# Kernel optimization log

Measured on AMD Instinct MI355X. Metric: run time of the kernel, lower is better.

## Reference

```python
import jax, jax.numpy as jnp
import numpy as np
import math

N_HEAD = 12
N_EMBD = 768

def setup_inputs() -> dict:
    key = jax.random.key(0)
    ks = jax.random.split(key, 5)
    B, T, C = 4, 2048, N_EMBD
    s_attn = 1.0 / math.sqrt(C)
    return {
        "x": jax.random.normal(ks[0], (B, T, C), jnp.float32),
        "w_attn": jax.random.normal(ks[1], (C, 3 * C), jnp.float32) * s_attn,
        "b_attn": jnp.zeros((3 * C,), jnp.float32),
        "w_proj": jax.random.normal(ks[2], (C, C), jnp.float32) * s_attn,
        "b_proj": jnp.zeros((C,), jnp.float32),
    }

def reference(x, w_attn, b_attn, w_proj, b_proj):
    B, T, C = x.shape
    H = N_HEAD
    D = C // H
    qkv = x @ w_attn + b_attn  # [B,T,3C]
    q, k, v = jnp.split(qkv, 3, axis=-1)
    # [B,T,C] -> [B,H,T,D]
    q = q.reshape(B, T, H, D).transpose(0, 2, 1, 3)
    k = k.reshape(B, T, H, D).transpose(0, 2, 1, 3)
    v = v.reshape(B, T, H, D).transpose(0, 2, 1, 3)
    att = jnp.einsum('bhqd,bhkd->bhqk', q, k) * (1.0 / math.sqrt(D))
    causal = jnp.tril(jnp.ones((T, T), bool))
    att = jnp.where(causal[None, None], att, -jnp.inf)
    att = jax.nn.softmax(att, axis=-1)
    y = jnp.einsum('bhqk,bhkd->bhqd', att, v)  # [B,H,T,D]
    y = y.transpose(0, 2, 1, 3).reshape(B, T, C)
    return y @ w_proj + b_proj
```

## Files before the change

kernel.cpp:

```cpp
#include <hip/hip_runtime.h>
#include <hip/hip_bf16.h>

typedef unsigned short u16;
typedef __attribute__((ext_vector_type(4))) short bf16x4;
typedef __attribute__((ext_vector_type(8))) short bf16x8;
typedef __attribute__((ext_vector_type(4))) float f32x4;
typedef __attribute__((ext_vector_type(16))) float f32x16;

#define NB_ 4
#define NT_ 2048
#define NC_ 768
#define NH_ 12
#define ND_ 64
#define NM_ (NB_*NT_)
#define KC_ 24

#define SCQ_ 0.18033688011112042f

__device__ __forceinline__ u16 f2bf(float f){
  union { float f; unsigned u; } c; c.f = f;
  unsigned u = c.u;
  return (u16)((u + 0x7fffu + ((u>>16)&1u)) >> 16);
}

__device__ __forceinline__ unsigned pkbf(float a, float b){
  __hip_bfloat162 h = __float22bfloat162_rn(make_float2(a,b));
  union { __hip_bfloat162 h; unsigned u; } c; c.h = h; return c.u;
}

__device__ __forceinline__ f32x16 mfma32(bf16x8 a, bf16x8 b, f32x16 c){
  return __builtin_amdgcn_mfma_f32_32x32x16_bf16(a, b, c, 0, 0, 0);
}

__device__ __forceinline__ void gload_lds16(const void* g, void* l){
  __builtin_amdgcn_global_load_lds(
    (const __attribute__((address_space(1))) void*)g,
    (__attribute__((address_space(3))) void*)l, 16, 0, 0);
}


__global__ __launch_bounds__(256) void cast_f32_bf16_k(
    const float* __restrict__ in, u16* __restrict__ out, int n4){
  int i = blockIdx.x*256 + threadIdx.x;
  if (i >= n4) return;
  float4 v = ((const float4*)in)[i];
  int row = i / (NC_/4), k4 = (i % (NC_/4))*4;
  size_t off = (((size_t)(row>>7)*KC_ + (k4>>5))*4 + ((k4>>3)&3))*1024 + (row&127)*8 + (k4&7);
  bf16x4 o;
  o[0]=(short)f2bf(v.x); o[1]=(short)f2bf(v.y);
  o[2]=(short)f2bf(v.z); o[3]=(short)f2bf(v.w);
  *(bf16x4*)(out + off) = o;
}

__global__ __launch_bounds__(256) void transpose_cast_k(
    const float* __restrict__ in, u16* __restrict__ out, int R, int Cc){
  __shared__ float tile[32][33];
  int tx = threadIdx.x, ty = threadIdx.y;
  int c0 = blockIdx.x*32, r0 = blockIdx.y*32;
  #pragma unroll
  for (int j=0;j<32;j+=8) tile[ty+j][tx] = in[(size_t)(r0+ty+j)*Cc + c0+tx];
  __syncthreads();
  #pragma unroll
  for (int j=0;j<32;j+=8){
    int n = c0+ty+j, k = r0+tx;
    size_t off = (((size_t)(n>>8)*KC_ + (k>>5))*4 + ((k>>3)&3))*2048 + (n&255)*8 + (k&7);
    out[off] = f2bf(tile[tx][ty+j]);
  }
}

template<int MODE>
__global__ __launch_bounds__(256,2) void gemm256(
  const u16* __restrict__ A, const u16* __restrict__ BT, const float* __restrict__ bias,
  u16* __restrict__ qo, u16* __restrict__ ko, u16* __restrict__ vo,
  float* __restrict__ fo)
{
  __shared__ u16 lds[2][4096 + 8192];
  const int t = threadIdx.x, w = t>>6, l = t&63;
  const int lq = l&31, h = l>>5;
  const int NXB = (MODE==0) ? 9 : 3;
  const int nwg = 64*NXB;
  int sw = (blockIdx.x & 7)*(nwg>>3) + (blockIdx.x >> 3);
  const int rb = sw / NXB, nb = sw % NXB;
  const int brow = rb*128, bcol = nb*256;
  const int wc = w*64;

  f32x16 acc[4][2];
  #pragma unroll
  for (int i=0;i<4;i++)
    #pragma unroll
    for (int j=0;j<2;j++)
      #pragma unroll
      for (int r=0;r<16;r++) acc[i][j][r] = 0.f;

  auto stage = [&](int buf, int kc){
    const u16* Ag = A  + ((size_t)(rb*KC_ + kc))*4096;
    const u16* Bg = BT + ((size_t)(nb*KC_ + kc))*8192;
    char* La = (char*)&lds[buf][0];
    char* Lb = (char*)&lds[buf][4096];
    #pragma unroll
    for (int it=0; it<2; ++it)
      gload_lds16(Ag + (it*256+t)*8, La + (it*256+t)*16);
    #pragma unroll
    for (int it=0; it<4; ++it)
      gload_lds16(Bg + (it*256+t)*8, Lb + (it*256+t)*16);
  };

  stage(0,0);
  __syncthreads();
  int cur = 0;
  for (int kc=0; kc<KC_; ++kc){
    if (kc+1 < KC_) stage(cur^1, kc+1);
    const u16* La = &lds[cur][0];
    const u16* Lb = &lds[cur][4096];
    #pragma unroll
    for (int ks=0; ks<2; ++ks){
      bf16x8 af[4], bfr[2];
      #pragma unroll
      for (int mi=0;mi<4;mi++)
        af[mi] = *(const bf16x8*)(La + ((2*ks+h)*128 + mi*32 + lq)*8);
      #pragma unroll
      for (int nj=0;nj<2;nj++)
        bfr[nj] = *(const bf16x8*)(Lb + ((2*ks+h)*256 + wc + nj*32 + lq)*8);
      __builtin_amdgcn_s_setprio(1);
      #pragma unroll
      for (int mi=0;mi<4;mi++)
        #pragma unroll
        for (int nj=0;nj<2;nj++)
          acc[mi][nj] = mfma32(af[mi], bfr[nj], acc[mi][nj]);
      __builtin_amdgcn_s_setprio(0);
    }
    __syncthreads();
    cur ^= 1;
  }

  if (MODE == 1){
    #pragma unroll
    for (int nj=0;nj<2;nj++){
      int n = bcol + wc + nj*32 + lq;
      float bs = bias[n];
      #pragma unroll
      for (int mi=0;mi<4;mi++)
        #pragma unroll
        for (int r=0;r<16;r++){
          int m = brow + mi*32 + (r&3) + 8*(r>>2) + 4*h;
          fo[(size_t)m*NC_ + n] = acc[mi][nj][r] + bs;
        }
    }
  } else {
    const int sec = nb/3;
    u16* outp = (sec==0) ? qo : (sec==1 ? ko : vo);
    #pragma unroll
    for (int nj=0;nj<2;nj++){
      int n = bcol + wc + nj*32 + lq;
      int cc = n - sec*NC_;
      int hd = cc >> 6, d = cc & 63;
      float bs = bias[n];
      #pragma unroll
      for (int mi=0;mi<4;mi++)
        #pragma unroll
        for (int r=0;r<16;r++){
          int m = brow + mi*32 + (r&3) + 8*(r>>2) + 4*h;
          int bb = m >> 11, tt = m & 2047;
          float v = acc[mi][nj][r] + bs;
          if (sec == 0) v *= SCQ_;
          size_t bhbase = ((size_t)bb*NH_ + hd)*((size_t)NT_*ND_);
          size_t off;
          if (sec == 0){
            off = bhbase + (size_t)tt*ND_ + d;
          } else if (sec == 1){
            off = bhbase + (size_t)(tt>>6)*4096 + (size_t)(d>>3)*512 + (tt&63)*8 + (d&7);
          } else {
            int p = (tt & ~15) | (h<<3) | (r&3) | (((r>>2)&1)<<2);
            off = bhbase + (size_t)(p>>6)*4096 + (size_t)((p&63)>>3)*512 + d*8 + (p&7);
          }
          outp[off] = f2bf(v);
        }
    }
  }
}

__global__ __launch_bounds__(256,4) void attn_kernel(
    const u16* __restrict__ qg, const u16* __restrict__ kg,
    const u16* __restrict__ vg, u16* __restrict__ y)
{
  __shared__ u16 lds[2][8192];
  const int t = threadIdx.x, w = t>>6, l = t&63;
  const int lq = l&31, h = l>>5;
  const int bid = blockIdx.x;
  const int qt = 15 - (bid/48);
  const int bh = bid % 48;
  const int bb = bh / NH_, hh = bh % NH_;
  const u16* qp = qg + (size_t)bh*NT_*ND_;
  const u16* kp = kg + (size_t)bh*NT_*ND_;
  const u16* vp = vg + (size_t)bh*ND_*NT_;
  const int qmin = qt*128 + w*32;
  const int q = qmin + lq;

  bf16x8 Qf[4];
  {
    const u16* qr = qp + (size_t)q*ND_ + 8*h;
    #pragma unroll
    for (int ks=0; ks<4; ++ks) Qf[ks] = *(const bf16x8*)(qr + ks*16);
  }

  f32x16 o0, o1;
  float psum[16];
  #pragma unroll
  for (int r=0;r<16;r++){ o0[r]=0.f; o1[r]=0.f; psum[r]=0.f; }
  const int nc = 2*qt + 2;

  auto stage = [&](int buf, int c){
    const u16* kc = kp + c*4096;
    const u16* vc = vp + c*4096;
    #pragma unroll
    for (int it=0; it<2; ++it){
      gload_lds16(kc + (it*256 + t)*8, (char*)&lds[buf][0]    + (it*256 + t)*16);
      gload_lds16(vc + (it*256 + t)*8, (char*)&lds[buf][4096] + (it*256 + t)*16);
    }
  };

  stage(0,0);
  __syncthreads();
  int cur = 0;
  for (int c=0; c<nc; ++c){
    if (c+1 < nc) stage(cur^1, c+1);
    const u16* Kb = &lds[cur][0];
    const u16* Vb = &lds[cur][4096];
    const int kv0 = c*64;

    f32x16 s0, s1;
    #pragma unroll
    for (int r=0;r<16;r++){ s0[r]=0.f; s1[r]=0.f; }
    __builtin_amdgcn_s_setprio(1);
    #pragma unroll
    for (int ks=0; ks<4; ++ks){
      bf16x8 k0 = *(const bf16x8*)(Kb + ((2*ks+h)*64      + lq)*8);
      bf16x8 k1 = *(const bf16x8*)(Kb + ((2*ks+h)*64 + 32 + lq)*8);
      s0 = mfma32(k0, Qf[ks], s0);
      s1 = mfma32(k1, Qf[ks], s1);
    }
    __builtin_amdgcn_s_setprio(0);

    if (kv0 + 63 > qmin){
      #pragma unroll
      for (int r=0;r<16;r++){
        int kva = kv0 + (r&3) + 8*(r>>2) + 4*h;
        s0[r] = (kva      <= q) ? s0[r] : -3e38f;
        s1[r] = (kva + 32 <= q) ? s1[r] : -3e38f;
      }
    }

    union { unsigned wd[16]; bf16x8 v[4]; } pf;
    #pragma unroll
    for (int j=0;j<8;j++){
      float a = exp2f(s0[2*j]), b = exp2f(s0[2*j+1]);
      psum[j] += a + b;
      pf.wd[j] = pkbf(a,b);
    }
    #pragma unroll
    for (int j=0;j<8;j++){
      float a = exp2f(s1[2*j]), b = exp2f(s1[2*j+1]);
      psum[8+j] += a + b;
      pf.wd[8+j] = pkbf(a,b);
    }

    __builtin_amdgcn_s_setprio(1);
    #pragma unroll
    for (int j=0;j<4;j++){
      bf16x8 v0 = *(const bf16x8*)(Vb + ((2*j+h)*64      + lq)*8);
      bf16x8 v1 = *(const bf16x8*)(Vb + ((2*j+h)*64 + 32 + lq)*8);
      o0 = mfma32(v0, pf.v[j], o0);
      o1 = mfma32(v1, pf.v[j], o1);
    }
    __builtin_amdgcn_s_setprio(0);
    __syncthreads();
    cur ^= 1;
  }

  #pragma unroll
  for (int st=8; st>=1; st>>=1)
    #pragma unroll
    for (int i=0;i<st;i++) psum[i] += psum[i+st];
  float lsum = psum[0] + __shfl_xor(psum[0], 32);
  float inv = 1.f / lsum;

  const int m = bb*NT_ + q;
  const int rbm = m>>7, rr = m&127;
  #pragma unroll
  for (int db=0; db<2; ++db){
    #pragma unroll
    for (int g2=0; g2<4; ++g2){
      float e0 = (db ? o1[g2*4+0] : o0[g2*4+0]) * inv;
      float e1 = (db ? o1[g2*4+1] : o0[g2*4+1]) * inv;
      float e2 = (db ? o1[g2*4+2] : o0[g2*4+2]) * inv;
      float e3 = (db ? o1[g2*4+3] : o0[g2*4+3]) * inv;
      unsigned w0 = pkbf(e0,e1), w1 = pkbf(e2,e3);
      int k = hh*ND_ + db*32 + g2*8 + 4*h;
      size_t off = (((size_t)rbm*KC_ + (k>>5))*4 + ((k>>3)&3))*1024 + rr*8 + (k&7);
      *(uint2*)(y + off) = make_uint2(w0, w1);
    }
  }
}

extern "C" void kernel_launch(void* const* d_in, const int* in_sizes, int n_in,
                              void* d_out, int out_size, void* d_ws, size_t ws_size,
                              hipStream_t stream) {
  const float* x  = (const float*)d_in[0];
  const float* wa = (const float*)d_in[1];
  const float* ba = (const float*)d_in[2];
  const float* wp = (const float*)d_in[3];
  const float* bp = (const float*)d_in[4];
  float* out = (float*)d_out;

  char* ws = (char*)d_ws;
  const size_t szXB = (size_t)NM_*NC_*2;
  const size_t szWA = (size_t)3*NC_*NC_*2;
  const size_t szWP = (size_t)NC_*NC_*2;
  const size_t szQ  = szXB;
  u16* xb  = (u16*)(ws);
  u16* wat = (u16*)(ws + szXB);
  u16* wpt = (u16*)(ws + szXB + szWA);
  u16* qb  = (u16*)(ws + szXB + szWA + szWP);
  u16* kb  = (u16*)((char*)qb + szQ);
  u16* vb  = (u16*)((char*)kb + szQ);
  u16* yb  = xb;

  cast_f32_bf16_k<<<dim3((NM_*NC_/4 + 255)/256), dim3(256), 0, stream>>>(x, xb, NM_*NC_/4);
  transpose_cast_k<<<dim3(3*NC_/32, NC_/32), dim3(32,8), 0, stream>>>(wa, wat, NC_, 3*NC_);
  transpose_cast_k<<<dim3(NC_/32, NC_/32), dim3(32,8), 0, stream>>>(wp, wpt, NC_, NC_);
  gemm256<0><<<dim3(64*9), dim3(256), 0, stream>>>(xb, wat, ba, qb, kb, vb, (float*)nullptr);
  attn_kernel<<<dim3(NB_*NH_*(NT_/128)), dim3(256), 0, stream>>>(qb, kb, vb, yb);
  gemm256<1><<<dim3(64*3), dim3(256), 0, stream>>>(yb, wpt, bp,
      (u16*)nullptr, (u16*)nullptr, (u16*)nullptr, out);
}
```

Baseline: 143.3 us.

## Use 128x128 GEMM tiles and triple-buffered LDS pipelines in GEMM and attention

```diff
diff --git a/kernel.cpp b/kernel.cpp
--- a/kernel.cpp
+++ b/kernel.cpp
@@ -63,30 +63,30 @@
   #pragma unroll
   for (int j=0;j<32;j+=8){
     int n = c0+ty+j, k = r0+tx;
-    size_t off = (((size_t)(n>>8)*KC_ + (k>>5))*4 + ((k>>3)&3))*2048 + (n&255)*8 + (k&7);
+    size_t off = (((size_t)(n>>7)*KC_ + (k>>5))*4 + ((k>>3)&3))*1024 + (n&127)*8 + (k&7);
     out[off] = f2bf(tile[tx][ty+j]);
   }
 }
 
 template<int MODE>
-__global__ __launch_bounds__(256,2) void gemm256(
+__global__ __launch_bounds__(256,3) void gemm128p(
   const u16* __restrict__ A, const u16* __restrict__ BT, const float* __restrict__ bias,
   u16* __restrict__ qo, u16* __restrict__ ko, u16* __restrict__ vo,
   float* __restrict__ fo)
 {
-  __shared__ u16 lds[2][4096 + 8192];
+  __shared__ u16 lds[3][8192];
   const int t = threadIdx.x, w = t>>6, l = t&63;
   const int lq = l&31, h = l>>5;
-  const int NXB = (MODE==0) ? 9 : 3;
+  const int NXB = (MODE==0) ? 18 : 6;
   const int nwg = 64*NXB;
   int sw = (blockIdx.x & 7)*(nwg>>3) + (blockIdx.x >> 3);
   const int rb = sw / NXB, nb = sw % NXB;
-  const int brow = rb*128, bcol = nb*256;
-  const int wc = w*64;
-
-  f32x16 acc[4][2];
-  #pragma unroll
-  for (int i=0;i<4;i++)
+  const int brow = rb*128, bcol = nb*128;
+  const int wr = (w>>1)*64, wc = (w&1)*64;
+
+  f32x16 acc[2][2];
+  #pragma unroll
+  for (int i=0;i<2;i++)
     #pragma unroll
     for (int j=0;j<2;j++)
       #pragma unroll
@@ -94,43 +94,43 @@
 
   auto stage = [&](int buf, int kc){
     const u16* Ag = A  + ((size_t)(rb*KC_ + kc))*4096;
-    const u16* Bg = BT + ((size_t)(nb*KC_ + kc))*8192;
+    const u16* Bg = BT + ((size_t)(nb*KC_ + kc))*4096;
     char* La = (char*)&lds[buf][0];
     char* Lb = (char*)&lds[buf][4096];
     #pragma unroll
-    for (int it=0; it<2; ++it)
+    for (int it=0; it<2; ++it){
       gload_lds16(Ag + (it*256+t)*8, La + (it*256+t)*16);
-    #pragma unroll
-    for (int it=0; it<4; ++it)
       gload_lds16(Bg + (it*256+t)*8, Lb + (it*256+t)*16);
+    }
   };
 
   stage(0,0);
-  __syncthreads();
+  stage(1,1);
   int cur = 0;
   for (int kc=0; kc<KC_; ++kc){
-    if (kc+1 < KC_) stage(cur^1, kc+1);
+    if (kc+1 < KC_) asm volatile("s_waitcnt vmcnt(4)\ns_barrier" ::: "memory");
+    else            asm volatile("s_waitcnt vmcnt(0)\ns_barrier" ::: "memory");
+    if (kc+2 < KC_){ int nb3 = cur+2; if (nb3>=3) nb3-=3; stage(nb3, kc+2); }
     const u16* La = &lds[cur][0];
     const u16* Lb = &lds[cur][4096];
     #pragma unroll
     for (int ks=0; ks<2; ++ks){
-      bf16x8 af[4], bfr[2];
-      #pragma unroll
-      for (int mi=0;mi<4;mi++)
-        af[mi] = *(const bf16x8*)(La + ((2*ks+h)*128 + mi*32 + lq)*8);
+      bf16x8 af[2], bfr[2];
+      #pragma unroll
+      for (int mi=0;mi<2;mi++)
+        af[mi]  = *(const bf16x8*)(La + ((2*ks+h)*128 + wr + mi*32 + lq)*8);
       #pragma unroll
       for (int nj=0;nj<2;nj++)
-        bfr[nj] = *(const bf16x8*)(Lb + ((2*ks+h)*256 + wc + nj*32 + lq)*8);
+        bfr[nj] = *(const bf16x8*)(Lb + ((2*ks+h)*128 + wc + nj*32 + lq)*8);
       __builtin_amdgcn_s_setprio(1);
       #pragma unroll
-      for (int mi=0;mi<4;mi++)
+      for (int mi=0;mi<2;mi++)
         #pragma unroll
         for (int nj=0;nj<2;nj++)
           acc[mi][nj] = mfma32(af[mi], bfr[nj], acc[mi][nj]);
       __builtin_amdgcn_s_setprio(0);
     }
-    __syncthreads();
-    cur ^= 1;
+    if (++cur == 3) cur = 0;
   }
 
   if (MODE == 1){
@@ -139,15 +139,15 @@
       int n = bcol + wc + nj*32 + lq;
       float bs = bias[n];
       #pragma unroll
-      for (int mi=0;mi<4;mi++)
+      for (int mi=0;mi<2;mi++)
         #pragma unroll
         for (int r=0;r<16;r++){
-          int m = brow + mi*32 + (r&3) + 8*(r>>2) + 4*h;
+          int m = brow + wr + mi*32 + (r&3) + 8*(r>>2) + 4*h;
           fo[(size_t)m*NC_ + n] = acc[mi][nj][r] + bs;
         }
     }
   } else {
-    const int sec = nb/3;
+    const int sec = nb/6;
     u16* outp = (sec==0) ? qo : (sec==1 ? ko : vo);
     #pragma unroll
     for (int nj=0;nj<2;nj++){
@@ -156,10 +156,10 @@
       int hd = cc >> 6, d = cc & 63;
       float bs = bias[n];
       #pragma unroll
-      for (int mi=0;mi<4;mi++)
+      for (int mi=0;mi<2;mi++)
         #pragma unroll
         for (int r=0;r<16;r++){
-          int m = brow + mi*32 + (r&3) + 8*(r>>2) + 4*h;
+          int m = brow + wr + mi*32 + (r&3) + 8*(r>>2) + 4*h;
           int bb = m >> 11, tt = m & 2047;
           float v = acc[mi][nj][r] + bs;
           if (sec == 0) v *= SCQ_;
@@ -179,11 +179,11 @@
   }
 }
 
-__global__ __launch_bounds__(256,4) void attn_kernel(
+__global__ __launch_bounds__(256,3) void attn_kernel(
     const u16* __restrict__ qg, const u16* __restrict__ kg,
     const u16* __restrict__ vg, u16* __restrict__ y)
 {
-  __shared__ u16 lds[2][8192];
+  __shared__ u16 lds[3][8192];
   const int t = threadIdx.x, w = t>>6, l = t&63;
   const int lq = l&31, h = l>>5;
   const int bid = blockIdx.x;
@@ -210,20 +210,22 @@
   const int nc = 2*qt + 2;
 
   auto stage = [&](int buf, int c){
-    const u16* kc = kp + c*4096;
-    const u16* vc = vp + c*4096;
+    const u16* kc2 = kp + c*4096;
+    const u16* vc2 = vp + c*4096;
     #pragma unroll
     for (int it=0; it<2; ++it){
-      gload_lds16(kc + (it*256 + t)*8, (char*)&lds[buf][0]    + (it*256 + t)*16);
-      gload_lds16(vc + (it*256 + t)*8, (char*)&lds[buf][4096] + (it*256 + t)*16);
+      gload_lds16(kc2 + (it*256 + t)*8, (char*)&lds[buf][0]    + (it*256 + t)*16);
+      gload_lds16(vc2 + (it*256 + t)*8, (char*)&lds[buf][4096] + (it*256 + t)*16);
     }
   };
 
   stage(0,0);
-  __syncthreads();
+  stage(1,1);
   int cur = 0;
   for (int c=0; c<nc; ++c){
-    if (c+1 < nc) stage(cur^1, c+1);
+    if (c+1 < nc) asm volatile("s_waitcnt vmcnt(4)\ns_barrier" ::: "memory");
+    else          asm volatile("s_waitcnt vmcnt(0)\ns_barrier" ::: "memory");
+    if (c+2 < nc){ int nb3 = cur+2; if (nb3>=3) nb3-=3; stage(nb3, c+2); }
     const u16* Kb = &lds[cur][0];
     const u16* Vb = &lds[cur][4096];
     const int kv0 = c*64;
@@ -273,8 +275,7 @@
       o1 = mfma32(v1, pf.v[j], o1);
     }
     __builtin_amdgcn_s_setprio(0);
-    __syncthreads();
-    cur ^= 1;
+    if (++cur == 3) cur = 0;
   }
 
   #pragma unroll
@@ -328,8 +329,8 @@
   cast_f32_bf16_k<<<dim3((NM_*NC_/4 + 255)/256), dim3(256), 0, stream>>>(x, xb, NM_*NC_/4);
   transpose_cast_k<<<dim3(3*NC_/32, NC_/32), dim3(32,8), 0, stream>>>(wa, wat, NC_, 3*NC_);
   transpose_cast_k<<<dim3(NC_/32, NC_/32), dim3(32,8), 0, stream>>>(wp, wpt, NC_, NC_);
-  gemm256<0><<<dim3(64*9), dim3(256), 0, stream>>>(xb, wat, ba, qb, kb, vb, (float*)nullptr);
+  gemm128p<0><<<dim3(64*18), dim3(256), 0, stream>>>(xb, wat, ba, qb, kb, vb, (float*)nullptr);
   attn_kernel<<<dim3(NB_*NH_*(NT_/128)), dim3(256), 0, stream>>>(qb, kb, vb, yb);
-  gemm256<1><<<dim3(64*3), dim3(256), 0, stream>>>(yb, wpt, bp,
+  gemm128p<1><<<dim3(64*6), dim3(256), 0, stream>>>(yb, wpt, bp,
       (u16*)nullptr, (u16*)nullptr, (u16*)nullptr, out);
 }
```

Result: faster. 131.9 us (-8.0%).
